# Kernel tuning notes

Hardware: AMD Instinct MI355X
Metric: run time of the kernel (lower is better)

Reference implementation:

```python
import jax, jax.numpy as jnp
import numpy as np
import math

B, S, HID, H = 1, 512, 256, 8
D = HID // H
SCALE = 1.0 / math.sqrt(D)
PI = math.pi


def setup_inputs() -> dict:
    key = jax.random.key(0)
    ks = jax.random.split(key, 6)
    x = jax.random.normal(ks[0], (B, S, HID), dtype=jnp.float32)
    w = lambda k: jax.random.normal(k, (HID, HID), dtype=jnp.float32) * 0.02
    return {
        'x': x,
        'wq': w(ks[1]), 'bq': jnp.zeros((HID,), jnp.float32),
        'wk': w(ks[2]), 'bk': jnp.zeros((HID,), jnp.float32),
        'wv': w(ks[3]), 'bv': jnp.zeros((HID,), jnp.float32),
        'wo': w(ks[4]), 'bo': jnp.zeros((HID,), jnp.float32),
    }


def _split_heads(t):
    # [B,S,HID] -> [B,H,S,D]
    return t.reshape(B, S, H, D).transpose(0, 2, 1, 3)


def reference(x, wq, bq, wk, bk, wv, bv, wo, bo):
    # Linear projections (torch nn.Linear: x @ W.T + b)
    q = _split_heads(x @ wq.T + bq)
    k = _split_heads(x @ wk.T + bk)
    v = _split_heads(x @ wv.T + bv)

    omega = jax.nn.sigmoid(q) * PI      # [B,H,S,D]
    amplitude = jax.nn.sigmoid(k)       # [B,H,S,D]
    phase = jnp.tanh(v) * PI            # [B,H,S,D]

    # relative position i-j, [S,S]
    pos = (jnp.arange(S)[:, None] - jnp.arange(S)[None, :]).astype(jnp.float32)
    # wave interference tensor [B,H,S,D,S] (query i, dim d, key j)
    interaction = amplitude[..., None] * jnp.cos(
        omega[..., None] * pos[None, None, :, None, :] + phase[..., None])
    patterns = jax.nn.softmax(interaction * SCALE, axis=-1)  # softmax over keys j
    # contract over key positions: per-dim attention
    context = jnp.einsum('bhidj,bhjd->bhid', patterns, v)    # [B,H,S,D]
    context = context.transpose(0, 2, 1, 3).reshape(B, S, HID)
    return context @ wo.T + bo
```

## Files before the change

### kernel.cpp

```cpp
#include <hip/hip_runtime.h>
#include <math.h>

#define SEQ 512
#define HID 256
#define NH 8
#define DH 32
#define PI_F 3.14159265358979323846f
#define SCALE_F 0.17677669529663687f
#define LOG2E_F 1.4426950408889634f

#define OFF_OMEGA 0
#define OFF_AMP   131072
#define OFF_PHASE 262144
#define OFF_V     393216
#define OFF_CTX   524288

__global__ __launch_bounds__(256) void gemm_qkv_act(
    const float* __restrict__ x,
    const float* __restrict__ wq, const float* __restrict__ bq,
    const float* __restrict__ wk, const float* __restrict__ bk,
    const float* __restrict__ wv, const float* __restrict__ bv,
    float* __restrict__ ws)
{
    const int b = blockIdx.x;
    const int which = b >> 6;
    const int t = b & 63;
    const int r0 = (t >> 3) * 64;
    const int c0 = (t & 7) * 32;
    const float* W = (which == 0) ? wq : (which == 1) ? wk : wv;
    const float* B = (which == 0) ? bq : (which == 1) ? bk : bv;

    __shared__ float xs[64][68];
    __shared__ float wls[32][68];

    const int tid = threadIdx.x;
    const int rg = tid >> 4, cg = tid & 15;

    float acc[4][2];
#pragma unroll
    for (int i = 0; i < 4; i++) { acc[i][0] = 0.f; acc[i][1] = 0.f; }

    for (int k0 = 0; k0 < HID; k0 += 64) {
#pragma unroll
        for (int it = 0; it < 4; it++) {
            int idx = tid + it * 256;
            int rr = idx >> 4, f = idx & 15;
            *(float4*)&xs[rr][4 * f] =
                *(const float4*)(x + (r0 + rr) * HID + k0 + 4 * f);
        }
#pragma unroll
        for (int it = 0; it < 2; it++) {
            int idx = tid + it * 256;
            int cc = idx >> 4, f = idx & 15;
            *(float4*)&wls[cc][4 * f] =
                *(const float4*)(W + (c0 + cc) * HID + k0 + 4 * f);
        }
        __syncthreads();
#pragma unroll
        for (int g = 0; g < 16; g++) {
            float4 wv0 = *(const float4*)&wls[2 * cg + 0][4 * g];
            float4 wv1 = *(const float4*)&wls[2 * cg + 1][4 * g];
#pragma unroll
            for (int i = 0; i < 4; i++) {
                float4 xv = *(const float4*)&xs[4 * rg + i][4 * g];
                acc[i][0] = fmaf(xv.x, wv0.x, acc[i][0]);
                acc[i][0] = fmaf(xv.y, wv0.y, acc[i][0]);
                acc[i][0] = fmaf(xv.z, wv0.z, acc[i][0]);
                acc[i][0] = fmaf(xv.w, wv0.w, acc[i][0]);
                acc[i][1] = fmaf(xv.x, wv1.x, acc[i][1]);
                acc[i][1] = fmaf(xv.y, wv1.y, acc[i][1]);
                acc[i][1] = fmaf(xv.z, wv1.z, acc[i][1]);
                acc[i][1] = fmaf(xv.w, wv1.w, acc[i][1]);
            }
        }
        __syncthreads();
    }

    const float b0 = B[c0 + 2 * cg + 0];
    const float b1 = B[c0 + 2 * cg + 1];
#pragma unroll
    for (int i = 0; i < 4; i++) {
        int row = r0 + 4 * rg + i;
#pragma unroll
        for (int j = 0; j < 2; j++) {
            float val = acc[i][j] + (j ? b1 : b0);
            int o = row * HID + c0 + 2 * cg + j;
            if (which == 0) {
                ws[OFF_OMEGA + o] = PI_F / (1.f + expf(-val));
            } else if (which == 1) {
                ws[OFF_AMP + o] = 1.f / (1.f + expf(-val));
            } else {
                ws[OFF_V + o] = val;
                ws[OFF_PHASE + o] = PI_F * tanhf(val);
            }
        }
    }
}

__global__ __launch_bounds__(256) void gemm_out_bias(
    const float* __restrict__ ctx, const float* __restrict__ wo,
    const float* __restrict__ bo, float* __restrict__ out)
{
    const int b = blockIdx.x;
    const int r0 = (b >> 3) * 32;
    const int c0 = (b & 7) * 32;

    __shared__ float xs[32][68];
    __shared__ float wls[32][68];

    const int tid = threadIdx.x;
    const int rg = tid >> 4, cg = tid & 15;

    float acc[2][2];
    acc[0][0] = acc[0][1] = acc[1][0] = acc[1][1] = 0.f;

    for (int k0 = 0; k0 < HID; k0 += 64) {
#pragma unroll
        for (int it = 0; it < 2; it++) {
            int idx = tid + it * 256;
            int rr = idx >> 4, f = idx & 15;
            *(float4*)&xs[rr][4 * f] =
                *(const float4*)(ctx + (r0 + rr) * HID + k0 + 4 * f);
            *(float4*)&wls[rr][4 * f] =
                *(const float4*)(wo + (c0 + rr) * HID + k0 + 4 * f);
        }
        __syncthreads();
#pragma unroll
        for (int g = 0; g < 16; g++) {
            float4 wv0 = *(const float4*)&wls[2 * cg + 0][4 * g];
            float4 wv1 = *(const float4*)&wls[2 * cg + 1][4 * g];
#pragma unroll
            for (int i = 0; i < 2; i++) {
                float4 xv = *(const float4*)&xs[2 * rg + i][4 * g];
                acc[i][0] = fmaf(xv.x, wv0.x, acc[i][0]);
                acc[i][0] = fmaf(xv.y, wv0.y, acc[i][0]);
                acc[i][0] = fmaf(xv.z, wv0.z, acc[i][0]);
                acc[i][0] = fmaf(xv.w, wv0.w, acc[i][0]);
                acc[i][1] = fmaf(xv.x, wv1.x, acc[i][1]);
                acc[i][1] = fmaf(xv.y, wv1.y, acc[i][1]);
                acc[i][1] = fmaf(xv.z, wv1.z, acc[i][1]);
                acc[i][1] = fmaf(xv.w, wv1.w, acc[i][1]);
            }
        }
        __syncthreads();
    }

    const float b0 = bo[c0 + 2 * cg + 0];
    const float b1 = bo[c0 + 2 * cg + 1];
#pragma unroll
    for (int i = 0; i < 2; i++) {
        int row = r0 + 2 * rg + i;
        out[row * HID + c0 + 2 * cg + 0] = acc[i][0] + b0;
        out[row * HID + c0 + 2 * cg + 1] = acc[i][1] + b1;
    }
}

__global__ __launch_bounds__(256) void wave_attn(const float* __restrict__ ws,
                                                 float* __restrict__ ctx)
{
    const int h  = blockIdx.y;
    const int il = threadIdx.x >> 5;
    const int d  = threadIdx.x & 31;
    const int i  = blockIdx.x * 8 + il;
    const int col = h * DH + d;

    const float w  = ws[OFF_OMEGA + i * HID + col];
    const float aL = ws[OFF_AMP + i * HID + col] * (SCALE_F * LOG2E_F);
    const float ph = ws[OFF_PHASE + i * HID + col];
    const float* vcol = ws + OFF_V + col;

    float sw_, cw;
    sincosf(w, &sw_, &cw);
    float c2 = cw * cw - sw_ * sw_, s2 = 2.f * sw_ * cw;
    float c4 = c2 * c2 - s2 * s2,   s4 = 2.f * s2 * c2;

    float th0 = fmaf(w, (float)i, ph);
    float s0, cc0;
    sincosf(th0, &s0, &cc0);

    float pc[4], psn[4];
    pc[0] = cc0; psn[0] = s0;
#pragma unroll
    for (int k = 1; k < 4; k++) {
        float nc = pc[k - 1] * cw + psn[k - 1] * sw_;
        float ns = psn[k - 1] * cw - pc[k - 1] * sw_;
        pc[k] = nc; psn[k] = ns;
    }
    float p[4], q[4], den[4], num[4];
#pragma unroll
    for (int k = 0; k < 4; k++) {
        p[k] = aL * pc[k]; q[k] = aL * psn[k];
        den[k] = 0.f; num[k] = 0.f;
    }

#pragma unroll 4
    for (int t = 0; t < SEQ / 4; t++) {
        float v0 = vcol[(4 * t + 0) * HID];
        float v1 = vcol[(4 * t + 1) * HID];
        float v2v = vcol[(4 * t + 2) * HID];
        float v3 = vcol[(4 * t + 3) * HID];
        float e0 = __builtin_amdgcn_exp2f(p[0]);
        float e1 = __builtin_amdgcn_exp2f(p[1]);
        float e2 = __builtin_amdgcn_exp2f(p[2]);
        float e3 = __builtin_amdgcn_exp2f(p[3]);
        den[0] += e0; den[1] += e1; den[2] += e2; den[3] += e3;
        num[0] = fmaf(e0, v0, num[0]);
        num[1] = fmaf(e1, v1, num[1]);
        num[2] = fmaf(e2, v2v, num[2]);
        num[3] = fmaf(e3, v3, num[3]);
#pragma unroll
        for (int k = 0; k < 4; k++) {
            float np = p[k] * c4 + q[k] * s4;
            float nq = q[k] * c4 - p[k] * s4;
            p[k] = np; q[k] = nq;
        }
    }
    float denom = (den[0] + den[1]) + (den[2] + den[3]);
    float numer = (num[0] + num[1]) + (num[2] + num[3]);
    ctx[i * HID + col] = numer / denom;
}

extern "C" void kernel_launch(void* const* d_in, const int* in_sizes, int n_in,
                              void* d_out, int out_size, void* d_ws, size_t ws_size,
                              hipStream_t stream) {
    const float* x  = (const float*)d_in[0];
    const float* wq = (const float*)d_in[1];
    const float* bq = (const float*)d_in[2];
    const float* wk = (const float*)d_in[3];
    const float* bk = (const float*)d_in[4];
    const float* wv = (const float*)d_in[5];
    const float* bv = (const float*)d_in[6];
    const float* wo = (const float*)d_in[7];
    const float* bo = (const float*)d_in[8];

    float* ws = (float*)d_ws;

    hipLaunchKernelGGL(gemm_qkv_act, dim3(192), dim3(256), 0, stream,
                       x, wq, bq, wk, bk, wv, bv, ws);
    hipLaunchKernelGGL(wave_attn, dim3(SEQ / 8, NH), dim3(256), 0, stream,
                       ws, ws + OFF_CTX);
    hipLaunchKernelGGL(gemm_out_bias, dim3(128), dim3(256), 0, stream,
                       ws + OFF_CTX, wo, bo, (float*)d_out);
}
```

Before: 112.4 us.

## Fuse output projection into wave attention via per-head atomic accumulation

Removes the separate output-projection GEMM kernel. Each attention block now multiplies its per-head context slice by the matching slice of wo held in shared memory and accumulates into the output with atomicAdd. The output is pre-initialised with the bias inside the QKV kernel. The QKV GEMM also gains register prefetch of the next K-tile, overlapping global loads with compute. The trade-off is that each attention block now loads a 32KB wo slice, issues eight-way atomic contention per output element, and uses more shared memory and registers, which may lower occupancy.

Result: faster. 109.4 us (-2.7%).

```diff
diff --git a/kernel.cpp b/kernel.cpp
--- a/kernel.cpp
+++ b/kernel.cpp
@@ -13,14 +13,14 @@
 #define OFF_AMP   131072
 #define OFF_PHASE 262144
 #define OFF_V     393216
-#define OFF_CTX   524288
 
 __global__ __launch_bounds__(256) void gemm_qkv_act(
     const float* __restrict__ x,
     const float* __restrict__ wq, const float* __restrict__ bq,
     const float* __restrict__ wk, const float* __restrict__ bk,
     const float* __restrict__ wv, const float* __restrict__ bv,
-    float* __restrict__ ws)
+    const float* __restrict__ bo,
+    float* __restrict__ ws, float* __restrict__ out)
 {
     const int b = blockIdx.x;
     const int which = b >> 6;
@@ -36,26 +36,43 @@
     const int tid = threadIdx.x;
     const int rg = tid >> 4, cg = tid & 15;
 
+    {
+        int base = b * 256 + tid;
+        for (int idx = base; idx < SEQ * HID; idx += 192 * 256)
+            out[idx] = bo[idx & 255];
+    }
+
+    const int arr = tid >> 4, af = tid & 15;
+    float4 pa[4], pw[2];
+#pragma unroll
+    for (int it = 0; it < 4; it++)
+        pa[it] = *(const float4*)(x + (r0 + arr + it * 16) * HID + 4 * af);
+#pragma unroll
+    for (int it = 0; it < 2; it++)
+        pw[it] = *(const float4*)(W + (c0 + arr + it * 16) * HID + 4 * af);
+
     float acc[4][2];
 #pragma unroll
     for (int i = 0; i < 4; i++) { acc[i][0] = 0.f; acc[i][1] = 0.f; }
 
     for (int k0 = 0; k0 < HID; k0 += 64) {
 #pragma unroll
-        for (int it = 0; it < 4; it++) {
-            int idx = tid + it * 256;
-            int rr = idx >> 4, f = idx & 15;
-            *(float4*)&xs[rr][4 * f] =
-                *(const float4*)(x + (r0 + rr) * HID + k0 + 4 * f);
-        }
-#pragma unroll
-        for (int it = 0; it < 2; it++) {
-            int idx = tid + it * 256;
-            int cc = idx >> 4, f = idx & 15;
-            *(float4*)&wls[cc][4 * f] =
-                *(const float4*)(W + (c0 + cc) * HID + k0 + 4 * f);
-        }
+        for (int it = 0; it < 4; it++)
+            *(float4*)&xs[arr + it * 16][4 * af] = pa[it];
+#pragma unroll
+        for (int it = 0; it < 2; it++)
+            *(float4*)&wls[arr + it * 16][4 * af] = pw[it];
         __syncthreads();
+
+        if (k0 + 64 < HID) {
+#pragma unroll
+            for (int it = 0; it < 4; it++)
+                pa[it] = *(const float4*)(x + (r0 + arr + it * 16) * HID + k0 + 64 + 4 * af);
+#pragma unroll
+            for (int it = 0; it < 2; it++)
+                pw[it] = *(const float4*)(W + (c0 + arr + it * 16) * HID + k0 + 64 + 4 * af);
+        }
+
 #pragma unroll
         for (int g = 0; g < 16; g++) {
             float4 wv0 = *(const float4*)&wls[2 * cg + 0][4 * g];
@@ -97,72 +114,32 @@
     }
 }
 
-__global__ __launch_bounds__(256) void gemm_out_bias(
-    const float* __restrict__ ctx, const float* __restrict__ wo,
-    const float* __restrict__ bo, float* __restrict__ out)
+__global__ __launch_bounds__(256) void wave_attn_out(
+    const float* __restrict__ ws, const float* __restrict__ wo,
+    float* __restrict__ out)
 {
-    const int b = blockIdx.x;
-    const int r0 = (b >> 3) * 32;
-    const int c0 = (b & 7) * 32;
-
-    __shared__ float xs[32][68];
-    __shared__ float wls[32][68];
-
-    const int tid = threadIdx.x;
-    const int rg = tid >> 4, cg = tid & 15;
-
-    float acc[2][2];
-    acc[0][0] = acc[0][1] = acc[1][0] = acc[1][1] = 0.f;
-
-    for (int k0 = 0; k0 < HID; k0 += 64) {
-#pragma unroll
-        for (int it = 0; it < 2; it++) {
-            int idx = tid + it * 256;
-            int rr = idx >> 4, f = idx & 15;
-            *(float4*)&xs[rr][4 * f] =
-                *(const float4*)(ctx + (r0 + rr) * HID + k0 + 4 * f);
-            *(float4*)&wls[rr][4 * f] =
-                *(const float4*)(wo + (c0 + rr) * HID + k0 + 4 * f);
-        }
-        __syncthreads();
-#pragma unroll
-        for (int g = 0; g < 16; g++) {
-            float4 wv0 = *(const float4*)&wls[2 * cg + 0][4 * g];
-            float4 wv1 = *(const float4*)&wls[2 * cg + 1][4 * g];
-#pragma unroll
-            for (int i = 0; i < 2; i++) {
-                float4 xv = *(const float4*)&xs[2 * rg + i][4 * g];
-                acc[i][0] = fmaf(xv.x, wv0.x, acc[i][0]);
-                acc[i][0] = fmaf(xv.y, wv0.y, acc[i][0]);
-                acc[i][0] = fmaf(xv.z, wv0.z, acc[i][0]);
-                acc[i][0] = fmaf(xv.w, wv0.w, acc[i][0]);
-                acc[i][1] = fmaf(xv.x, wv1.x, acc[i][1]);
-                acc[i][1] = fmaf(xv.y, wv1.y, acc[i][1]);
-                acc[i][1] = fmaf(xv.z, wv1.z, acc[i][1]);
-                acc[i][1] = fmaf(xv.w, wv1.w, acc[i][1]);
-            }
-        }
-        __syncthreads();
-    }
-
-    const float b0 = bo[c0 + 2 * cg + 0];
-    const float b1 = bo[c0 + 2 * cg + 1];
-#pragma unroll
-    for (int i = 0; i < 2; i++) {
-        int row = r0 + 2 * rg + i;
-        out[row * HID + c0 + 2 * cg + 0] = acc[i][0] + b0;
-        out[row * HID + c0 + 2 * cg + 1] = acc[i][1] + b1;
-    }
-}
-
-__global__ __launch_bounds__(256) void wave_attn(const float* __restrict__ ws,
-                                                 float* __restrict__ ctx)
-{
-    const int h  = blockIdx.y;
+    const int b  = blockIdx.x;
+    const int i8 = b >> 3;
+    const int h  = b & 7;
     const int il = threadIdx.x >> 5;
     const int d  = threadIdx.x & 31;
-    const int i  = blockIdx.x * 8 + il;
+    const int i  = i8 * 8 + il;
     const int col = h * DH + d;
+    const int tid = threadIdx.x;
+
+    __shared__ float wo_l[256][33];
+    __shared__ float ctx_l[8][33];
+
+#pragma unroll
+    for (int it = 0; it < 8; it++) {
+        int idx = tid + it * 256;
+        int c = idx >> 3, f = idx & 7;
+        float4 wv = *(const float4*)(wo + c * HID + h * DH + 4 * f);
+        wo_l[c][4 * f + 0] = wv.x;
+        wo_l[c][4 * f + 1] = wv.y;
+        wo_l[c][4 * f + 2] = wv.z;
+        wo_l[c][4 * f + 3] = wv.w;
+    }
 
     const float w  = ws[OFF_OMEGA + i * HID + col];
     const float aL = ws[OFF_AMP + i * HID + col] * (SCALE_F * LOG2E_F);
@@ -217,7 +194,23 @@
     }
     float denom = (den[0] + den[1]) + (den[2] + den[3]);
     float numer = (num[0] + num[1]) + (num[2] + num[3]);
-    ctx[i * HID + col] = numer / denom;
+
+    __syncthreads();
+    ctx_l[il][d] = numer / denom;
+    __syncthreads();
+
+    float ctx_r[32];
+#pragma unroll
+    for (int kk = 0; kk < 32; kk++) ctx_r[kk] = ctx_l[il][kk];
+#pragma unroll
+    for (int m = 0; m < 8; m++) {
+        const int c = d + 32 * m;
+        float s = 0.f;
+#pragma unroll
+        for (int kk = 0; kk < 32; kk++)
+            s = fmaf(ctx_r[kk], wo_l[c][kk], s);
+        atomicAdd(&out[i * HID + c], s);
+    }
 }
 
 extern "C" void kernel_launch(void* const* d_in, const int* in_sizes, int n_in,
@@ -233,12 +226,11 @@
     const float* wo = (const float*)d_in[7];
     const float* bo = (const float*)d_in[8];
 
-    float* ws = (float*)d_ws;
+    float* ws  = (float*)d_ws;
+    float* out = (float*)d_out;
 
     hipLaunchKernelGGL(gemm_qkv_act, dim3(192), dim3(256), 0, stream,
-                       x, wq, bq, wk, bk, wv, bv, ws);
-    hipLaunchKernelGGL(wave_attn, dim3(SEQ / 8, NH), dim3(256), 0, stream,
-                       ws, ws + OFF_CTX);
-    hipLaunchKernelGGL(gemm_out_bias, dim3(128), dim3(256), 0, stream,
-                       ws + OFF_CTX, wo, bo, (float*)d_out);
+                       x, wq, bq, wk, bk, wv, bv, bo, ws, out);
+    hipLaunchKernelGGL(wave_attn_out, dim3(512), dim3(256), 0, stream,
+                       ws, wo, out);
 }
```
